# Performance work log

Hardware: AMD Instinct MI355X
Metric: run time of the kernel (lower is better)

## Reference

```python
import jax, jax.numpy as jnp
import numpy as np

N = 10000   # nodes (Hi-C bins)
E = 640000  # directed edges
H = 2       # attention heads
C = 512     # per-head out channels
NEG_SLOPE = 0.2

def _leaky_relu(v):
    return jnp.where(v >= 0, v, NEG_SLOPE * v)

def setup_inputs() -> dict:
    key = jax.random.key(0)
    ks = jax.random.split(key, 16)
    s = 0.02
    return {
        "x": jax.random.normal(ks[0], (N, 512), jnp.float32),
        "edge_index": jax.random.randint(ks[1], (2, E), 0, N, dtype=jnp.int64),
        "W": jax.random.normal(ks[2], (512, H * C), jnp.float32) * s,
        "att_src": jax.random.normal(ks[3], (H, C), jnp.float32) * s,
        "att_dst": jax.random.normal(ks[4], (H, C), jnp.float32) * s,
        "bias_conv": jnp.zeros((H * C,), jnp.float32),
        "Wa": jax.random.normal(ks[5], (1024, 256), jnp.float32) * s,
        "ba": jnp.zeros((256,), jnp.float32),
        "W1": jax.random.normal(ks[6], (256, 128), jnp.float32) * s,
        "b1": jnp.zeros((128,), jnp.float32),
        "W2": jax.random.normal(ks[7], (128, 64), jnp.float32) * s,
        "b2": jnp.zeros((64,), jnp.float32),
        "W3": jax.random.normal(ks[8], (64, 3), jnp.float32) * s,
        "b3": jnp.zeros((3,), jnp.float32),
    }

def reference(x, edge_index, W, att_src, att_dst, bias_conv,
              Wa, ba, W1, b1, W2, b2, W3, b3):
    n = x.shape[0]
    # PyG GATConv default: add self loops
    loop = jnp.arange(n, dtype=edge_index.dtype)
    src = jnp.concatenate([edge_index[0], loop])  # [E+N]
    dst = jnp.concatenate([edge_index[1], loop])
    # linear projection -> [N, H, C]
    h = (x @ W).reshape(n, H, C)
    a_src = jnp.einsum('nhc,hc->nh', h, att_src)  # [N, H]
    a_dst = jnp.einsum('nhc,hc->nh', h, att_dst)
    e = _leaky_relu(a_src[src] + a_dst[dst])      # [E+N, H]
    # segment softmax over destination nodes
    m = jax.ops.segment_max(e, dst, num_segments=n)
    ex = jnp.exp(e - m[dst])
    denom = jax.ops.segment_sum(ex, dst, num_segments=n)
    alpha = ex / denom[dst]                        # [E+N, H]
    # weighted scatter-add aggregation
    out = jax.ops.segment_sum(h[src] * alpha[..., None], dst, num_segments=n)
    out = out.reshape(n, H * C) + bias_conv        # concat heads -> [N, 1024]
    # MLP (dropout is identity in eval)
    y = jax.nn.relu(out)
    y = jax.nn.relu(y @ Wa + ba)
    y = jax.nn.relu(y @ W1 + b1)
    y = jax.nn.relu(y @ W2 + b2)
    y = y @ W3 + b3                                # [N, 3]
    # cdist p=2 via gram trick, grad-safe sqrt at 0
    sq = jnp.sum(y * y, axis=1)
    d2 = jnp.maximum(sq[:, None] + sq[None, :] - 2.0 * (y @ y.T), 0.0)
    pos = d2 > 0
    return jnp.where(pos, jnp.sqrt(jnp.where(pos, d2, 1.0)), 0.0)  # [N, N]
```

## Files before the change

### kernel.cpp

```cpp
#include <hip/hip_runtime.h>
#include <hip/hip_bf16.h>
#include <math.h>

#define N_NODES 10000
#define NE      640000
#define NTOT    (NE + N_NODES)
#define HC      1024
#define CC      512

typedef __attribute__((ext_vector_type(8))) short bf16x8;
typedef __attribute__((ext_vector_type(4))) float f32x4;

__device__ __forceinline__ float lrelu(float v) { return v >= 0.f ? v : 0.2f * v; }

__device__ __forceinline__ void split1(float f, ushort& h, ushort& l) {
    unsigned u = __float_as_uint(f);
    unsigned hb = (u + 0x7FFFu + ((u >> 16) & 1u)) >> 16;
    float fh = __uint_as_float(hb << 16);
    float fl = f - fh;
    unsigned ul = __float_as_uint(fl);
    unsigned lb = (ul + 0x7FFFu + ((ul >> 16) & 1u)) >> 16;
    h = (ushort)hb; l = (ushort)lb;
}

__global__ __launch_bounds__(256) void split_bf16(
    const float* __restrict__ in, ushort* __restrict__ hi,
    ushort* __restrict__ lo, int n4)
{
    int i = blockIdx.x * blockDim.x + threadIdx.x;
    if (i >= n4) return;
    float4 v = *(const float4*)(in + (size_t)i * 4);
    float vv[4] = {v.x, v.y, v.z, v.w};
    ushort hh[4], ll[4];
    #pragma unroll
    for (int j = 0; j < 4; ++j) split1(vv[j], hh[j], ll[j]);
    *(ushort4*)(hi + (size_t)i * 4) = make_ushort4(hh[0], hh[1], hh[2], hh[3]);
    *(ushort4*)(lo + (size_t)i * 4) = make_ushort4(ll[0], ll[1], ll[2], ll[3]);
}

__global__ __launch_bounds__(256) void transp_split(
    const float* __restrict__ Win, int K, int N,
    ushort* __restrict__ Th, ushort* __restrict__ Tl)
{
    __shared__ float tile[32][33];
    int n0 = blockIdx.x * 32, k0 = blockIdx.y * 32;
    int tx = threadIdx.x & 31, ty = threadIdx.x >> 5;
    #pragma unroll
    for (int r = 0; r < 4; ++r)
        tile[ty + r * 8][tx] = Win[(size_t)(k0 + ty + r * 8) * N + n0 + tx];
    __syncthreads();
    #pragma unroll
    for (int r = 0; r < 4; ++r) {
        int n = ty + r * 8;
        float f = tile[tx][n];
        ushort h, l;
        split1(f, h, l);
        Th[(size_t)(n0 + n) * K + k0 + tx] = h;
        Tl[(size_t)(n0 + n) * K + k0 + tx] = l;
    }
}

template<int RELU_BIAS>
__global__ __launch_bounds__(256) void gemm_bf16x3(
    const ushort* __restrict__ Ah, const ushort* __restrict__ Al,
    const ushort* __restrict__ Bh, const ushort* __restrict__ Bl,
    const float* __restrict__ biasC,
    float* __restrict__ C, int M, int N, int K)
{
    __shared__ __align__(16) ushort sAh[4][128][8];
    __shared__ __align__(16) ushort sAl[4][128][8];
    __shared__ __align__(16) ushort sBh[4][128][8];
    __shared__ __align__(16) ushort sBl[4][128][8];
    const int bm = blockIdx.y * 128;
    const int bn = blockIdx.x * 128;
    const int tid = threadIdx.x;
    const int lane = tid & 63;
    const int w = tid >> 6;
    const int wm = (w >> 1) * 64, wn = (w & 1) * 64;
    const int l15 = lane & 15, l4 = lane >> 4;

    f32x4 acc[4][4];
    #pragma unroll
    for (int i = 0; i < 4; ++i)
        #pragma unroll
        for (int j = 0; j < 4; ++j)
            acc[i][j] = (f32x4){0.f, 0.f, 0.f, 0.f};

    for (int k0 = 0; k0 < K; k0 += 32) {
        #pragma unroll
        for (int qi = 0; qi < 4; ++qi) {
            int Q = qi * 256 + tid;
            int m = Q >> 3;
            int kq = (Q & 7) * 4;
            int gr = bm + m;
            ushort4 vh = make_ushort4(0, 0, 0, 0), vl = vh;
            if (gr < M) {
                vh = *(const ushort4*)(Ah + (size_t)gr * K + k0 + kq);
                vl = *(const ushort4*)(Al + (size_t)gr * K + k0 + kq);
            }
            *(ushort4*)&sAh[kq >> 3][m][kq & 7] = vh;
            *(ushort4*)&sAl[kq >> 3][m][kq & 7] = vl;
            ushort4 wh = *(const ushort4*)(Bh + (size_t)(bn + m) * K + k0 + kq);
            ushort4 wl = *(const ushort4*)(Bl + (size_t)(bn + m) * K + k0 + kq);
            *(ushort4*)&sBh[kq >> 3][m][kq & 7] = wh;
            *(ushort4*)&sBl[kq >> 3][m][kq & 7] = wl;
        }
        __syncthreads();
        bf16x8 ah[4], al[4], bh[4], bl[4];
        #pragma unroll
        for (int i = 0; i < 4; ++i) {
            ah[i] = *(const bf16x8*)&sAh[l4][wm + i * 16 + l15][0];
            al[i] = *(const bf16x8*)&sAl[l4][wm + i * 16 + l15][0];
            bh[i] = *(const bf16x8*)&sBh[l4][wn + i * 16 + l15][0];
            bl[i] = *(const bf16x8*)&sBl[l4][wn + i * 16 + l15][0];
        }
        #pragma unroll
        for (int i = 0; i < 4; ++i)
            #pragma unroll
            for (int j = 0; j < 4; ++j) {
                acc[i][j] = __builtin_amdgcn_mfma_f32_16x16x32_bf16(ah[i], bh[j], acc[i][j], 0, 0, 0);
                acc[i][j] = __builtin_amdgcn_mfma_f32_16x16x32_bf16(ah[i], bl[j], acc[i][j], 0, 0, 0);
                acc[i][j] = __builtin_amdgcn_mfma_f32_16x16x32_bf16(al[i], bh[j], acc[i][j], 0, 0, 0);
            }
        __syncthreads();
    }
    #pragma unroll
    for (int i = 0; i < 4; ++i) {
        #pragma unroll
        for (int r = 0; r < 4; ++r) {
            int row = bm + wm + i * 16 + l4 * 4 + r;
            if (row >= M) continue;
            #pragma unroll
            for (int j = 0; j < 4; ++j) {
                int col = bn + wn + j * 16 + l15;
                float v = acc[i][j][r];
                if (RELU_BIAS) v = fmaxf(v + biasC[col], 0.f);
                C[(size_t)row * N + col] = v;
            }
        }
    }
}

template<int ACT_IN, int RELU_OUT>
__global__ __launch_bounds__(256) void gemm64(
    const float* __restrict__ A, const float* __restrict__ biasA,
    const float* __restrict__ B, const float* __restrict__ biasC,
    float* __restrict__ C, int M, int N, int K)
{
    __shared__ float As[16][68];
    __shared__ float Bs[16][68];
    const int bm = blockIdx.y * 64;
    const int bn = blockIdx.x * 64;
    const int tid = threadIdx.x;
    const int tx = tid & 15, ty = tid >> 4;

    const int arow  = tid >> 2;
    const int acol4 = (tid & 3) * 4;
    const int brow  = tid >> 4;
    const int bcol4 = (tid & 15) * 4;

    float acc[4][4] = {};

    for (int k0 = 0; k0 < K; k0 += 16) {
        int gr = bm + arow;
        float4 av = make_float4(0.f, 0.f, 0.f, 0.f);
        if (gr < M) av = *(const float4*)(A + (size_t)gr * K + k0 + acol4);
        if (ACT_IN) {
            av.x = fmaxf(av.x + biasA[k0 + acol4 + 0], 0.f);
            av.y = fmaxf(av.y + biasA[k0 + acol4 + 1], 0.f);
            av.z = fmaxf(av.z + biasA[k0 + acol4 + 2], 0.f);
            av.w = fmaxf(av.w + biasA[k0 + acol4 + 3], 0.f);
        }
        As[acol4 + 0][arow] = av.x;
        As[acol4 + 1][arow] = av.y;
        As[acol4 + 2][arow] = av.z;
        As[acol4 + 3][arow] = av.w;
        float4 bv = *(const float4*)(B + (size_t)(k0 + brow) * N + bn + bcol4);
        *(float4*)&Bs[brow][bcol4] = bv;
        __syncthreads();
        #pragma unroll
        for (int k = 0; k < 16; ++k) {
            float a0 = As[k][ty * 4 + 0], a1 = As[k][ty * 4 + 1];
            float a2 = As[k][ty * 4 + 2], a3 = As[k][ty * 4 + 3];
            float b0 = Bs[k][tx * 4 + 0], b1 = Bs[k][tx * 4 + 1];
            float b2 = Bs[k][tx * 4 + 2], b3 = Bs[k][tx * 4 + 3];
            acc[0][0] += a0 * b0; acc[0][1] += a0 * b1; acc[0][2] += a0 * b2; acc[0][3] += a0 * b3;
            acc[1][0] += a1 * b0; acc[1][1] += a1 * b1; acc[1][2] += a1 * b2; acc[1][3] += a1 * b3;
            acc[2][0] += a2 * b0; acc[2][1] += a2 * b1; acc[2][2] += a2 * b2; acc[2][3] += a2 * b3;
            acc[3][0] += a3 * b0; acc[3][1] += a3 * b1; acc[3][2] += a3 * b2; acc[3][3] += a3 * b3;
        }
        __syncthreads();
    }
    #pragma unroll
    for (int i = 0; i < 4; ++i) {
        int row = bm + ty * 4 + i;
        if (row >= M) continue;
        #pragma unroll
        for (int j = 0; j < 4; ++j) {
            int col = bn + tx * 4 + j;
            float v = acc[i][j];
            if (biasC) v += biasC[col];
            if (RELU_OUT) v = fmaxf(v, 0.f);
            C[(size_t)row * N + col] = v;
        }
    }
}

__global__ __launch_bounds__(256) void att_dots(
    const float* __restrict__ h, const float* __restrict__ att_src,
    const float* __restrict__ att_dst, float* __restrict__ a_src,
    float* __restrict__ a_dst)
{
    int wave = threadIdx.x >> 6;
    int lane = threadIdx.x & 63;
    int p = blockIdx.x * 4 + wave;
    if (p >= N_NODES * 2) return;
    int n = p >> 1, hd = p & 1;
    const float* hp = h + (size_t)n * HC + hd * CC;
    const float* as = att_src + hd * CC;
    const float* ad = att_dst + hd * CC;
    float s1 = 0.f, s2 = 0.f;
    for (int c = lane; c < CC; c += 64) {
        float hv = hp[c];
        s1 += hv * as[c];
        s2 += hv * ad[c];
    }
    #pragma unroll
    for (int o = 32; o > 0; o >>= 1) {
        s1 += __shfl_xor(s1, o);
        s2 += __shfl_xor(s2, o);
    }
    if (lane == 0) { a_src[p] = s1; a_dst[p] = s2; }
}

__global__ __launch_bounds__(256) void count_deg(
    const int* __restrict__ ei, int* __restrict__ deg)
{
    int e = blockIdx.x * blockDim.x + threadIdx.x;
    if (e >= NTOT) return;
    int d = (e < NE) ? ei[NE + e] : e - NE;
    atomicAdd(&deg[d], 1);
}

__global__ __launch_bounds__(1024) void scan_deg(
    const int* __restrict__ deg, int* __restrict__ row_start)
{
    __shared__ int part[1024];
    int t = threadIdx.x;
    int base = t * 10;
    int local[10];
    int s = 0;
    #pragma unroll
    for (int j = 0; j < 10; ++j) { local[j] = deg[base + j]; s += local[j]; }
    part[t] = s;
    __syncthreads();
    for (int off = 1; off < 1024; off <<= 1) {
        int v = (t >= off) ? part[t - off] : 0;
        __syncthreads();
        part[t] += v;
        __syncthreads();
    }
    int run = (t == 0) ? 0 : part[t - 1];
    #pragma unroll
    for (int j = 0; j < 10; ++j) {
        if (base + j <= N_NODES) row_start[base + j] = run;
        run += local[j];
    }
}

__global__ __launch_bounds__(256) void scatter_edges(
    const int* __restrict__ ei, const int* __restrict__ row_start,
    int* __restrict__ cursor, int* __restrict__ srclist)
{
    int e = blockIdx.x * blockDim.x + threadIdx.x;
    if (e >= NTOT) return;
    int s, d;
    if (e < NE) { s = ei[e]; d = ei[NE + e]; } else { s = d = e - NE; }
    int pos = atomicAdd(&cursor[d], 1);
    srclist[row_start[d] + pos] = s;
}

__global__ __launch_bounds__(256) void seg_softmax_stats(
    const int* __restrict__ row_start, const int* __restrict__ srclist,
    const float2* __restrict__ a_src2, const float* __restrict__ a_dst,
    int2* __restrict__ pack0, int2* __restrict__ pack1,
    float* __restrict__ dinv)
{
    int wave = threadIdx.x >> 6;
    int lane = threadIdx.x & 63;
    int d = blockIdx.x * 4 + wave;
    if (d >= N_NODES) return;
    int beg = row_start[d], end = row_start[d + 1];
    float ad0 = a_dst[d * 2], ad1 = a_dst[d * 2 + 1];
    float s0 = 0.f, s1 = 0.f;
    for (int i = beg + lane; i < end; i += 64) {
        int s = srclist[i];
        float2 a = a_src2[s];
        float e0 = expf(lrelu(a.x + ad0));
        float e1 = expf(lrelu(a.y + ad1));
        pack0[i] = make_int2(s, __float_as_int(e0));
        pack1[i] = make_int2(s, __float_as_int(e1));
        s0 += e0;
        s1 += e1;
    }
    #pragma unroll
    for (int o = 32; o > 0; o >>= 1) {
        s0 += __shfl_xor(s0, o);
        s1 += __shfl_xor(s1, o);
    }
    if (lane == 0) {
        dinv[d * 2 + 0] = 1.f / s0;
        dinv[d * 2 + 1] = 1.f / s1;
    }
}

__global__ __launch_bounds__(256) void aggregate_w4(
    const int* __restrict__ row_start,
    const int2* __restrict__ pack0, const int2* __restrict__ pack1,
    const float* __restrict__ dinv, const float* __restrict__ bias_conv,
    const float* __restrict__ h,
    ushort* __restrict__ outh, ushort* __restrict__ outl)
{
    int wave = threadIdx.x >> 6;
    int lane = threadIdx.x & 63;
    int g    = lane >> 4;
    int l16  = lane & 15;
    int d = blockIdx.x * 4 + wave;
    int chunk = blockIdx.y;
    int cb = chunk * 64;
    int hd = chunk >> 3;
    const int2* __restrict__ pk = (hd == 0) ? pack0 : pack1;
    int beg = row_start[d], end = row_start[d + 1];
    float inv = dinv[d * 2 + hd];
    const float* hbase = h + cb + l16 * 4;
    float4 ac0 = make_float4(0.f, 0.f, 0.f, 0.f);
    float4 ac1 = make_float4(0.f, 0.f, 0.f, 0.f);
    float4 ac2 = make_float4(0.f, 0.f, 0.f, 0.f);
    float4 ac3 = make_float4(0.f, 0.f, 0.f, 0.f);
    int i = beg + g;
    for (; i + 12 < end; i += 16) {
        int2 e0 = pk[i];
        int2 e1 = pk[i + 4];
        int2 e2 = pk[i + 8];
        int2 e3 = pk[i + 12];
        const float4 h0 = *(const float4*)(hbase + (size_t)e0.x * HC);
        const float4 h1 = *(const float4*)(hbase + (size_t)e1.x * HC);
        const float4 h2 = *(const float4*)(hbase + (size_t)e2.x * HC);
        const float4 h3 = *(const float4*)(hbase + (size_t)e3.x * HC);
        float a0 = __int_as_float(e0.y), a1 = __int_as_float(e1.y);
        float a2 = __int_as_float(e2.y), a3 = __int_as_float(e3.y);
        ac0.x += a0 * h0.x; ac0.y += a0 * h0.y; ac0.z += a0 * h0.z; ac0.w += a0 * h0.w;
        ac1.x += a1 * h1.x; ac1.y += a1 * h1.y; ac1.z += a1 * h1.z; ac1.w += a1 * h1.w;
        ac2.x += a2 * h2.x; ac2.y += a2 * h2.y; ac2.z += a2 * h2.z; ac2.w += a2 * h2.w;
        ac3.x += a3 * h3.x; ac3.y += a3 * h3.y; ac3.z += a3 * h3.z; ac3.w += a3 * h3.w;
    }
    for (; i < end; i += 4) {
        int2 e0 = pk[i];
        float a0 = __int_as_float(e0.y);
        const float4 h0 = *(const float4*)(hbase + (size_t)e0.x * HC);
        ac0.x += a0 * h0.x; ac0.y += a0 * h0.y; ac0.z += a0 * h0.z; ac0.w += a0 * h0.w;
    }
    ac0.x += ac1.x + ac2.x + ac3.x;
    ac0.y += ac1.y + ac2.y + ac3.y;
    ac0.z += ac1.z + ac2.z + ac3.z;
    ac0.w += ac1.w + ac2.w + ac3.w;
    ac0.x += __shfl_xor(ac0.x, 16); ac0.y += __shfl_xor(ac0.y, 16);
    ac0.z += __shfl_xor(ac0.z, 16); ac0.w += __shfl_xor(ac0.w, 16);
    ac0.x += __shfl_xor(ac0.x, 32); ac0.y += __shfl_xor(ac0.y, 32);
    ac0.z += __shfl_xor(ac0.z, 32); ac0.w += __shfl_xor(ac0.w, 32);
    if (g == 0) {
        int c0 = cb + l16 * 4;
        float v[4];
        v[0] = fmaxf(ac0.x * inv + bias_conv[c0 + 0], 0.f);
        v[1] = fmaxf(ac0.y * inv + bias_conv[c0 + 1], 0.f);
        v[2] = fmaxf(ac0.z * inv + bias_conv[c0 + 2], 0.f);
        v[3] = fmaxf(ac0.w * inv + bias_conv[c0 + 3], 0.f);
        ushort hh[4], ll[4];
        #pragma unroll
        for (int j = 0; j < 4; ++j) split1(v[j], hh[j], ll[j]);
        *(ushort4*)(outh + (size_t)d * HC + c0) = make_ushort4(hh[0], hh[1], hh[2], hh[3]);
        *(ushort4*)(outl + (size_t)d * HC + c0) = make_ushort4(ll[0], ll[1], ll[2], ll[3]);
    }
}

__global__ __launch_bounds__(256) void mlp3_sq(
    const float* __restrict__ y3, const float* __restrict__ W3,
    const float* __restrict__ b3, float* __restrict__ y, float* __restrict__ sq)
{
    int n = blockIdx.x * blockDim.x + threadIdx.x;
    if (n >= N_NODES) return;
    float acc0 = b3[0], acc1 = b3[1], acc2 = b3[2];
    const float* r = y3 + (size_t)n * 64;
    #pragma unroll 8
    for (int k = 0; k < 64; ++k) {
        float v = r[k];
        acc0 += v * W3[k * 3 + 0];
        acc1 += v * W3[k * 3 + 1];
        acc2 += v * W3[k * 3 + 2];
    }
    y[n * 3 + 0] = acc0; y[n * 3 + 1] = acc1; y[n * 3 + 2] = acc2;
    sq[n] = acc0 * acc0 + acc1 * acc1 + acc2 * acc2;
}

__global__ __launch_bounds__(256) void pdist(
    const float* __restrict__ y, const float* __restrict__ sq,
    float* __restrict__ out)
{
    int i = blockIdx.y;
    int j0 = (blockIdx.x * 256 + threadIdx.x) * 4;
    if (j0 >= N_NODES) return;
    float yi0 = y[i * 3 + 0], yi1 = y[i * 3 + 1], yi2 = y[i * 3 + 2];
    float si = sq[i];
    float res[4];
    #pragma unroll
    for (int t = 0; t < 4; ++t) {
        int j = j0 + t;
        float d2 = si + sq[j] - 2.f * (yi0 * y[j * 3 + 0] + yi1 * y[j * 3 + 1] + yi2 * y[j * 3 + 2]);
        d2 = fmaxf(d2, 0.f);
        res[t] = d2 > 0.f ? sqrtf(d2) : 0.f;
    }
    *(float4*)(out + (size_t)i * N_NODES + j0) = make_float4(res[0], res[1], res[2], res[3]);
}

extern "C" void kernel_launch(void* const* d_in, const int* in_sizes, int n_in,
                              void* d_out, int out_size, void* d_ws, size_t ws_size,
                              hipStream_t stream) {
    const float* x         = (const float*)d_in[0];
    const int*   ei        = (const int*)d_in[1];
    const float* W         = (const float*)d_in[2];
    const float* att_src   = (const float*)d_in[3];
    const float* att_dst   = (const float*)d_in[4];
    const float* bias_conv = (const float*)d_in[5];
    const float* Wa        = (const float*)d_in[6];
    const float* ba        = (const float*)d_in[7];
    const float* W1        = (const float*)d_in[8];
    const float* b1        = (const float*)d_in[9];
    const float* W2        = (const float*)d_in[10];
    const float* b2        = (const float*)d_in[11];
    const float* W3        = (const float*)d_in[12];
    const float* b3        = (const float*)d_in[13];
    float* out = (float*)d_out;

    float*  h        = out;
    ushort* outh     = (ushort*)(out + 10240000);
    ushort* outl     = (ushort*)(out + 15360000);
    float*  y1       = out + 20480000;
    float*  y2       = out + 23040000;
    float*  y3       = out + 24320000;
    float*  a_src    = out + 24960000;
    float*  a_dst    = out + 24980000;
    float*  dinv     = out + 25020000;
    int*    deg      = (int*)(out + 25040000);
    int*    row_st   = (int*)(out + 25060000);
    int*    cursor   = (int*)(out + 25080000);
    int*    srclist  = (int*)(out + 25100000);
    int2*   pack0    = (int2*)(out + 25760000);
    int2*   pack1    = (int2*)(out + 27060000);
    ushort* xh       = (ushort*)(out + 28360000);
    ushort* xl       = (ushort*)(out + 30920000);
    ushort* Wth      = (ushort*)(out + 33480000);
    ushort* Wtl      = (ushort*)(out + 33800000);
    ushort* Wath     = (ushort*)(out + 34120000);
    ushort* Watl     = (ushort*)(out + 34260000);

    float* y  = (float*)d_ws;
    float* sq = (float*)d_ws + 30000;

    hipMemsetAsync(deg, 0, 10240 * sizeof(int), stream);
    hipMemsetAsync(cursor, 0, 10240 * sizeof(int), stream);

    split_bf16<<<(N_NODES * 512 / 4 + 255) / 256, 256, 0, stream>>>(x, xh, xl, N_NODES * 512 / 4);
    transp_split<<<dim3(1024 / 32, 512 / 32), 256, 0, stream>>>(W, 512, 1024, Wth, Wtl);
    transp_split<<<dim3(256 / 32, 1024 / 32), 256, 0, stream>>>(Wa, 1024, 256, Wath, Watl);
    gemm_bf16x3<0><<<dim3(1024 / 128, (N_NODES + 127) / 128), 256, 0, stream>>>(
        xh, xl, Wth, Wtl, nullptr, h, N_NODES, 1024, 512);

    att_dots<<<(N_NODES * 2 + 3) / 4, 256, 0, stream>>>(h, att_src, att_dst, a_src, a_dst);

    count_deg<<<(NTOT + 255) / 256, 256, 0, stream>>>(ei, deg);
    scan_deg<<<1, 1024, 0, stream>>>(deg, row_st);
    scatter_edges<<<(NTOT + 255) / 256, 256, 0, stream>>>(ei, row_st, cursor, srclist);

    seg_softmax_stats<<<(N_NODES + 3) / 4, 256, 0, stream>>>(
        row_st, srclist, (const float2*)a_src, a_dst, pack0, pack1, dinv);

    aggregate_w4<<<dim3(N_NODES / 4, 16), 256, 0, stream>>>(
        row_st, pack0, pack1, dinv, bias_conv, h, outh, outl);

    gemm_bf16x3<1><<<dim3(256 / 128, (N_NODES + 127) / 128), 256, 0, stream>>>(
        outh, outl, Wath, Watl, ba, y1, N_NODES, 256, 1024);
    gemm64<0, 1><<<dim3(128 / 64, (N_NODES + 63) / 64), 256, 0, stream>>>(
        y1, nullptr, W1, b1, y2, N_NODES, 128, 256);
    gemm64<0, 1><<<dim3(64 / 64, (N_NODES + 63) / 64), 256, 0, stream>>>(
        y2, nullptr, W2, b2, y3, N_NODES, 64, 128);
    mlp3_sq<<<(N_NODES + 255) / 256, 256, 0, stream>>>(y3, W3, b3, y, sq);

    pdist<<<dim3((N_NODES + 1023) / 1024, N_NODES), 256, 0, stream>>>(y, sq, out);
}
```

Baseline: 564.1 us.

## Fuse attention dot products into projection GEMM and final MLP layer into gemm64

The attention-score dot products are computed in the epilogue of the first projection GEMM, using shuffle reductions and atomicAdd into zeroed a_src/a_dst buffers, so the separate att_dots pass that re-read h is removed. The last linear layer plus the squared-norm computation are folded into the epilogue of the W2 gemm64, which drops the y3 intermediate and the mlp3_sq kernel. The two memsets become one by placing deg and cursor next to the attention buffers. The cost is atomics in the GEMM epilogue and results that depend on atomic ordering.

```diff
diff --git a/kernel.cpp b/kernel.cpp
--- a/kernel.cpp
+++ b/kernel.cpp
@@ -60,11 +60,13 @@
     }
 }
 
-template<int RELU_BIAS>
+template<int RELU_BIAS, int ATT>
 __global__ __launch_bounds__(256) void gemm_bf16x3(
     const ushort* __restrict__ Ah, const ushort* __restrict__ Al,
     const ushort* __restrict__ Bh, const ushort* __restrict__ Bl,
     const float* __restrict__ biasC,
+    const float* __restrict__ attS, const float* __restrict__ attD,
+    float* __restrict__ aS, float* __restrict__ aD,
     float* __restrict__ C, int M, int N, int K)
 {
     __shared__ __align__(16) ushort sAh[4][128][8];
@@ -124,28 +126,48 @@
             }
         __syncthreads();
     }
+    const int head = ATT ? ((bn + wn) >> 9) : 0;
     #pragma unroll
     for (int i = 0; i < 4; ++i) {
         #pragma unroll
         for (int r = 0; r < 4; ++r) {
             int row = bm + wm + i * 16 + l4 * 4 + r;
             if (row >= M) continue;
+            float ps = 0.f, pd = 0.f;
             #pragma unroll
             for (int j = 0; j < 4; ++j) {
                 int col = bn + wn + j * 16 + l15;
                 float v = acc[i][j][r];
                 if (RELU_BIAS) v = fmaxf(v + biasC[col], 0.f);
                 C[(size_t)row * N + col] = v;
+                if (ATT) {
+                    int cc = col & (CC - 1);
+                    ps += v * attS[head * CC + cc];
+                    pd += v * attD[head * CC + cc];
+                }
+            }
+            if (ATT) {
+                #pragma unroll
+                for (int o = 1; o < 16; o <<= 1) {
+                    ps += __shfl_xor(ps, o);
+                    pd += __shfl_xor(pd, o);
+                }
+                if (l15 == 0) {
+                    atomicAdd(&aS[row * 2 + head], ps);
+                    atomicAdd(&aD[row * 2 + head], pd);
+                }
             }
         }
     }
 }
 
-template<int ACT_IN, int RELU_OUT>
+template<int RELU_OUT, int MLP3>
 __global__ __launch_bounds__(256) void gemm64(
-    const float* __restrict__ A, const float* __restrict__ biasA,
-    const float* __restrict__ B, const float* __restrict__ biasC,
-    float* __restrict__ C, int M, int N, int K)
+    const float* __restrict__ A, const float* __restrict__ B,
+    const float* __restrict__ biasC, float* __restrict__ C,
+    const float* __restrict__ W3, const float* __restrict__ b3,
+    float* __restrict__ y, float* __restrict__ sq,
+    int M, int N, int K)
 {
     __shared__ float As[16][68];
     __shared__ float Bs[16][68];
@@ -165,12 +187,6 @@
         int gr = bm + arow;
         float4 av = make_float4(0.f, 0.f, 0.f, 0.f);
         if (gr < M) av = *(const float4*)(A + (size_t)gr * K + k0 + acol4);
-        if (ACT_IN) {
-            av.x = fmaxf(av.x + biasA[k0 + acol4 + 0], 0.f);
-            av.y = fmaxf(av.y + biasA[k0 + acol4 + 1], 0.f);
-            av.z = fmaxf(av.z + biasA[k0 + acol4 + 2], 0.f);
-            av.w = fmaxf(av.w + biasA[k0 + acol4 + 3], 0.f);
-        }
         As[acol4 + 0][arow] = av.x;
         As[acol4 + 1][arow] = av.y;
         As[acol4 + 2][arow] = av.z;
@@ -195,42 +211,37 @@
     for (int i = 0; i < 4; ++i) {
         int row = bm + ty * 4 + i;
         if (row >= M) continue;
-        #pragma unroll
-        for (int j = 0; j < 4; ++j) {
-            int col = bn + tx * 4 + j;
-            float v = acc[i][j];
-            if (biasC) v += biasC[col];
-            if (RELU_OUT) v = fmaxf(v, 0.f);
-            C[(size_t)row * N + col] = v;
+        if (MLP3) {
+            float p0 = 0.f, p1 = 0.f, p2 = 0.f;
+            #pragma unroll
+            for (int j = 0; j < 4; ++j) {
+                int col = tx * 4 + j;
+                float v = fmaxf(acc[i][j] + biasC[col], 0.f);
+                p0 += v * W3[col * 3 + 0];
+                p1 += v * W3[col * 3 + 1];
+                p2 += v * W3[col * 3 + 2];
+            }
+            #pragma unroll
+            for (int o = 1; o < 16; o <<= 1) {
+                p0 += __shfl_xor(p0, o);
+                p1 += __shfl_xor(p1, o);
+                p2 += __shfl_xor(p2, o);
+            }
+            if (tx == 0) {
+                p0 += b3[0]; p1 += b3[1]; p2 += b3[2];
+                y[row * 3 + 0] = p0; y[row * 3 + 1] = p1; y[row * 3 + 2] = p2;
+                sq[row] = p0 * p0 + p1 * p1 + p2 * p2;
+            }
+        } else {
+            #pragma unroll
+            for (int j = 0; j < 4; ++j) {
+                int col = bn + tx * 4 + j;
+                float v = acc[i][j] + biasC[col];
+                if (RELU_OUT) v = fmaxf(v, 0.f);
+                C[(size_t)row * N + col] = v;
+            }
         }
     }
-}
-
-__global__ __launch_bounds__(256) void att_dots(
-    const float* __restrict__ h, const float* __restrict__ att_src,
-    const float* __restrict__ att_dst, float* __restrict__ a_src,
-    float* __restrict__ a_dst)
-{
-    int wave = threadIdx.x >> 6;
-    int lane = threadIdx.x & 63;
-    int p = blockIdx.x * 4 + wave;
-    if (p >= N_NODES * 2) return;
-    int n = p >> 1, hd = p & 1;
-    const float* hp = h + (size_t)n * HC + hd * CC;
-    const float* as = att_src + hd * CC;
-    const float* ad = att_dst + hd * CC;
-    float s1 = 0.f, s2 = 0.f;
-    for (int c = lane; c < CC; c += 64) {
-        float hv = hp[c];
-        s1 += hv * as[c];
-        s2 += hv * ad[c];
-    }
-    #pragma unroll
-    for (int o = 32; o > 0; o >>= 1) {
-        s1 += __shfl_xor(s1, o);
-        s2 += __shfl_xor(s2, o);
-    }
-    if (lane == 0) { a_src[p] = s1; a_dst[p] = s2; }
 }
 
 __global__ __launch_bounds__(256) void count_deg(
@@ -383,25 +394,6 @@
     }
 }
 
-__global__ __launch_bounds__(256) void mlp3_sq(
-    const float* __restrict__ y3, const float* __restrict__ W3,
-    const float* __restrict__ b3, float* __restrict__ y, float* __restrict__ sq)
-{
-    int n = blockIdx.x * blockDim.x + threadIdx.x;
-    if (n >= N_NODES) return;
-    float acc0 = b3[0], acc1 = b3[1], acc2 = b3[2];
-    const float* r = y3 + (size_t)n * 64;
-    #pragma unroll 8
-    for (int k = 0; k < 64; ++k) {
-        float v = r[k];
-        acc0 += v * W3[k * 3 + 0];
-        acc1 += v * W3[k * 3 + 1];
-        acc2 += v * W3[k * 3 + 2];
-    }
-    y[n * 3 + 0] = acc0; y[n * 3 + 1] = acc1; y[n * 3 + 2] = acc2;
-    sq[n] = acc0 * acc0 + acc1 * acc1 + acc2 * acc2;
-}
-
 __global__ __launch_bounds__(256) void pdist(
     const float* __restrict__ y, const float* __restrict__ sq,
     float* __restrict__ out)
@@ -446,13 +438,12 @@
     ushort* outl     = (ushort*)(out + 15360000);
     float*  y1       = out + 20480000;
     float*  y2       = out + 23040000;
-    float*  y3       = out + 24320000;
     float*  a_src    = out + 24960000;
     float*  a_dst    = out + 24980000;
-    float*  dinv     = out + 25020000;
-    int*    deg      = (int*)(out + 25040000);
+    int*    deg      = (int*)(out + 25000000);
+    int*    cursor   = (int*)(out + 25010240);
+    float*  dinv     = out + 25040000;
     int*    row_st   = (int*)(out + 25060000);
-    int*    cursor   = (int*)(out + 25080000);
     int*    srclist  = (int*)(out + 25100000);
     int2*   pack0    = (int2*)(out + 25760000);
     int2*   pack1    = (int2*)(out + 27060000);
@@ -466,16 +457,13 @@
     float* y  = (float*)d_ws;
     float* sq = (float*)d_ws + 30000;
 
-    hipMemsetAsync(deg, 0, 10240 * sizeof(int), stream);
-    hipMemsetAsync(cursor, 0, 10240 * sizeof(int), stream);
+    hipMemsetAsync(a_src, 0, (size_t)60480 * sizeof(float), stream);
 
     split_bf16<<<(N_NODES * 512 / 4 + 255) / 256, 256, 0, stream>>>(x, xh, xl, N_NODES * 512 / 4);
     transp_split<<<dim3(1024 / 32, 512 / 32), 256, 0, stream>>>(W, 512, 1024, Wth, Wtl);
     transp_split<<<dim3(256 / 32, 1024 / 32), 256, 0, stream>>>(Wa, 1024, 256, Wath, Watl);
-    gemm_bf16x3<0><<<dim3(1024 / 128, (N_NODES + 127) / 128), 256, 0, stream>>>(
-        xh, xl, Wth, Wtl, nullptr, h, N_NODES, 1024, 512);
-
-    att_dots<<<(N_NODES * 2 + 3) / 4, 256, 0, stream>>>(h, att_src, att_dst, a_src, a_dst);
+    gemm_bf16x3<0, 1><<<dim3(1024 / 128, (N_NODES + 127) / 128), 256, 0, stream>>>(
+        xh, xl, Wth, Wtl, nullptr, att_src, att_dst, a_src, a_dst, h, N_NODES, 1024, 512);
 
     count_deg<<<(NTOT + 255) / 256, 256, 0, stream>>>(ei, deg);
     scan_deg<<<1, 1024, 0, stream>>>(deg, row_st);
@@ -487,13 +475,12 @@
     aggregate_w4<<<dim3(N_NODES / 4, 16), 256, 0, stream>>>(
         row_st, pack0, pack1, dinv, bias_conv, h, outh, outl);
 
-    gemm_bf16x3<1><<<dim3(256 / 128, (N_NODES + 127) / 128), 256, 0, stream>>>(
-        outh, outl, Wath, Watl, ba, y1, N_NODES, 256, 1024);
-    gemm64<0, 1><<<dim3(128 / 64, (N_NODES + 63) / 64), 256, 0, stream>>>(
-        y1, nullptr, W1, b1, y2, N_NODES, 128, 256);
-    gemm64<0, 1><<<dim3(64 / 64, (N_NODES + 63) / 64), 256, 0, stream>>>(
-        y2, nullptr, W2, b2, y3, N_NODES, 64, 128);
-    mlp3_sq<<<(N_NODES + 255) / 256, 256, 0, stream>>>(y3, W3, b3, y, sq);
+    gemm_bf16x3<1, 0><<<dim3(256 / 128, (N_NODES + 127) / 128), 256, 0, stream>>>(
+        outh, outl, Wath, Watl, ba, nullptr, nullptr, nullptr, nullptr, y1, N_NODES, 256, 1024);
+    gemm64<1, 0><<<dim3(128 / 64, (N_NODES + 63) / 64), 256, 0, stream>>>(
+        y1, W1, b1, y2, nullptr, nullptr, nullptr, nullptr, N_NODES, 128, 256);
+    gemm64<1, 1><<<dim3(1, (N_NODES + 63) / 64), 256, 0, stream>>>(
+        y2, W2, b2, nullptr, W3, b3, y, sq, N_NODES, 64, 128);
 
     pdist<<<dim3((N_NODES + 1023) / 1024, N_NODES), 256, 0, stream>>>(y, sq, out);
 }
```

Result: no change. 558.6 us (-1.0%).
